# Kernel tuning notes

Measured on AMD Instinct MI355X. Metric: run time of the kernel, lower is better.

Reference implementation:

```python
import jax, jax.numpy as jnp
import numpy as np

B, L, C, H = 1, 2048, 2048, 16
D = C // H
EPS = 1e-6
W0 = 30.0  # SIREN frequency

def rmsnorm(x, w, eps=EPS):
    return x * jax.lax.rsqrt(jnp.mean(x * x, axis=-1, keepdims=True) + eps) * w

def depth_rope(x, depth, base=10000.0):
    # same rotation for all positions, angle set by scalar layer depth
    d = x.shape[-1]
    half = d // 2
    freqs = 1.0 / base ** (jnp.arange(half, dtype=x.dtype) / half)
    ang = depth * freqs
    cos, sin = jnp.cos(ang), jnp.sin(ang)
    x1, x2 = x[..., :half], x[..., half:2 * half]
    return jnp.concatenate([x1 * cos - x2 * sin, x1 * sin + x2 * cos], axis=-1)

def setup_inputs() -> dict:
    key = jax.random.key(0)
    ks = jax.random.split(key, 13)
    s = 1.0 / np.sqrt(C)
    inp = {
        'x':  jax.random.normal(ks[0], (B, L, C), jnp.float32),
        'h0': jax.random.normal(ks[1], (B, L, C), jnp.float32),
        'h1': jax.random.normal(ks[2], (B, L, C), jnp.float32),
        'h2': jax.random.normal(ks[3], (B, L, C), jnp.float32),
        'Wq': jax.random.normal(ks[4], (C, C), jnp.float32) * s,
        'Wk': jax.random.normal(ks[5], (C, C), jnp.float32) * s,
        'Wv': jax.random.normal(ks[6], (C, C), jnp.float32) * s,
        'Wo': jax.random.normal(ks[7], (C, C), jnp.float32) * s,
        'qn_w': jnp.ones((D,), jnp.float32),
        'kn_w': jnp.ones((D,), jnp.float32),
        'on_w': jnp.ones((C,), jnp.float32),
        'sw1': jax.random.normal(ks[8], (1, C), jnp.float32),
        'sb1': jax.random.normal(ks[9], (C,), jnp.float32) * 0.01,
        'sw2': jax.random.normal(ks[10], (C, C), jnp.float32) * s,
        'sb2': jnp.zeros((C,), jnp.float32),
    }
    return inp

def reference(x, h0, h1, h2, Wq, Wk, Wv, Wo, qn_w, kn_w, on_w, sw1, sb1, sw2, sb2):
    history = [h0, h1, h2]
    q_src = history[-1]                      # [B,L,C]
    q_depth = len(history) - 1
    # Q path: proj -> per-head RMSNorm -> depth RoPE
    q = jnp.einsum('blc,oc->blo', q_src, Wq).reshape(B, L, H, D)
    q = depth_rope(rmsnorm(q, qn_w), q_depth)
    # K/V path over prior history entries (each with its own depth)
    k_parts, v_parts = [], []
    for depth_idx, kv in enumerate(history[:-1]):
        k_i = jnp.einsum('blc,oc->blo', kv, Wk).reshape(B, L, H, D)
        v_i = jnp.einsum('blc,oc->blo', kv, Wv).reshape(B, L, H, D)
        k_parts.append(depth_rope(rmsnorm(k_i, kn_w), depth_idx))
        v_parts.append(v_i)
    k = jnp.concatenate(k_parts, axis=1)     # [B,Lkv,H,D]
    v = jnp.concatenate(v_parts, axis=1)
    # full SDPA, default scale D^-0.5
    scores = jnp.einsum('bqhd,bkhd->bhqk', q, k) * (D ** -0.5)
    attn = jax.nn.softmax(scores, axis=-1)
    out = jnp.einsum('bhqk,bkhd->bqhd', attn, v).reshape(B, L, C)
    out = jnp.einsum('blc,oc->blo', out, Wo)
    # SIREN upsample to (L,): target length == L -> identity interpolation
    # plus sine-activated coordinate MLP (implicit positional field)
    coords = jnp.linspace(-1.0, 1.0, L, dtype=x.dtype)[:, None]   # [L,1]
    pos = jnp.sin(W0 * (coords @ sw1 + sb1)) @ sw2 + sb2           # [L,C]
    out = out + pos[None]
    return x + rmsnorm(out, on_w)
```

## Files before the change

### kernel.cpp

```cpp
#include <hip/hip_runtime.h>
#include <hip/hip_fp16.h>

#define LQ 2048
#define CDIM 2048
#define NHEAD 16
#define HDIM 128
#define LKEY 4096

typedef _Float16 f16x8 __attribute__((ext_vector_type(8)));
typedef _Float16 f16x4 __attribute__((ext_vector_type(4)));
typedef float f32x4 __attribute__((ext_vector_type(4)));

#define GLOAD_LDS16(g, s) __builtin_amdgcn_global_load_lds( \
    (const __attribute__((address_space(1))) void*)(g),     \
    (__attribute__((address_space(3))) void*)(s), 16, 0, 0)

#define MFMA16(a, b, c) __builtin_amdgcn_mfma_f32_16x16x32_f16(a, b, c, 0, 0, 0)

__device__ __forceinline__ void storeC(float* p, float v) { *p = v; }
__device__ __forceinline__ void storeC(__half* p, float v) { *p = __float2half(v); }

template <int MODE, typename OutT>
__device__ __forceinline__ void gemm_body(
    __half* smem,
    const __half* __restrict__ A, const __half* __restrict__ B,
    OutT* __restrict__ C, int lda, int ldb, int ldc, int K,
    int bmA, int bmC, int bn,
    const float* __restrict__ wgt, int kmode, float oscale,
    __half* __restrict__ vTo)
{
    __half* lA = smem;
    __half* lB = smem + 8192;
    const int tid  = threadIdx.x;
    const int lane = tid & 63;
    const int wave = tid >> 6;
    const int r = tid >> 3;
    const int g = tid & 7;
    const __half* gA = A + (long)(bmA * 128 + r) * lda + ((g ^ (r & 7)) << 3);
    const __half* gB = B + (long)(bn * 128 + r) * ldb + ((g ^ (r & 7)) << 3);
    __half* lAp = lA + tid * 8;
    __half* lBp = lB + tid * 8;
    const int wr = (wave & 1) << 6;
    const int wc = (wave >> 1) << 6;
    const int l15 = lane & 15, quad = lane >> 4;

    f32x4 acc[4][4] = {};

    for (int kt = 0; kt < K; kt += 64) {
#pragma unroll
        for (int i = 0; i < 4; ++i) {
            GLOAD_LDS16(gA + (long)i * 32 * lda, lAp + i * 2048);
            GLOAD_LDS16(gB + (long)i * 32 * ldb, lBp + i * 2048);
        }
        gA += 64; gB += 64;
        __syncthreads();
#pragma unroll
        for (int kk = 0; kk < 2; ++kk) {
            f16x8 af[4], bfr[4];
#pragma unroll
            for (int mi = 0; mi < 4; ++mi) {
                const int m = wr + mi * 16 + l15;
                const int kg = kk * 4 + quad;
                af[mi] = *(const f16x8*)&lA[m * 64 + ((kg ^ (m & 7)) << 3)];
            }
#pragma unroll
            for (int ni = 0; ni < 4; ++ni) {
                const int n = wc + ni * 16 + l15;
                const int kg = kk * 4 + quad;
                bfr[ni] = *(const f16x8*)&lB[n * 64 + ((kg ^ (n & 7)) << 3)];
            }
#pragma unroll
            for (int mi = 0; mi < 4; ++mi)
#pragma unroll
                for (int ni = 0; ni < 4; ++ni)
                    acc[mi][ni] = MFMA16(af[mi], bfr[ni], acc[mi][ni]);
        }
        __syncthreads();
    }

    if constexpr (MODE == 0) {
        const int row0 = bmC * 128 + wr + quad * 4;
        const int col0 = bn * 128 + wc + l15;
#pragma unroll
        for (int mi = 0; mi < 4; ++mi)
#pragma unroll
            for (int ni = 0; ni < 4; ++ni)
#pragma unroll
                for (int rx = 0; rx < 4; ++rx)
                    storeC(&C[(long)(row0 + mi * 16 + rx) * ldc + col0 + ni * 16],
                           acc[mi][ni][rx]);
    } else if constexpr (MODE == 2) {
#pragma unroll
        for (int mi = 0; mi < 4; ++mi)
#pragma unroll
            for (int ni = 0; ni < 4; ++ni)
#pragma unroll
                for (int rx = 0; rx < 4; ++rx) {
                    const int  d   = (bn - 16) * 128 + wc + ni * 16 + l15;
                    const long key = (long)bmC * 128 + wr + mi * 16 + quad * 4 + rx;
                    vTo[(long)d * LKEY + key] = __float2half(acc[mi][ni][rx]);
                }
    } else {
        __half* sT = smem;
#pragma unroll
        for (int mi = 0; mi < 4; ++mi)
#pragma unroll
            for (int ni = 0; ni < 4; ++ni)
#pragma unroll
                for (int rx = 0; rx < 4; ++rx)
                    sT[(wr + mi * 16 + quad * 4 + rx) * 136 + wc + ni * 16 + l15] =
                        (_Float16)acc[mi][ni][rx];
        __syncthreads();
        const int row = (wave << 5) + (lane >> 1);
        const int c0  = (lane & 1) << 5;
        const __half* rp = sT + row * 136;
        f16x8 L[4], Hh[4];
#pragma unroll
        for (int j8 = 0; j8 < 4; ++j8) {
            L[j8]  = *(const f16x8*)&rp[c0 + j8 * 8];
            Hh[j8] = *(const f16x8*)&rp[c0 + 64 + j8 * 8];
        }
        float ss = 0.f;
#pragma unroll
        for (int j8 = 0; j8 < 4; ++j8)
#pragma unroll
            for (int e = 0; e < 8; ++e) {
                const float a = (float)L[j8][e], b = (float)Hh[j8][e];
                ss += a * a + b * b;
            }
        ss += __shfl_xor(ss, 1);
        const float rn = rsqrtf(ss * (1.0f / 128.0f) + 1e-6f);
        const long grow = (long)bmC * 128 + row;
        const int depth = kmode ? (grow < 2048 ? 0 : 1) : 2;
        union { f16x8 v; _Float16 e[8]; } o1[4], o2[4];
#pragma unroll
        for (int j8 = 0; j8 < 4; ++j8)
#pragma unroll
            for (int e = 0; e < 8; ++e) {
                const int d = c0 + j8 * 8 + e;
                const float x1 = (float)L[j8][e]  * rn * wgt[d];
                const float x2 = (float)Hh[j8][e] * rn * wgt[d + 64];
                const float ang = (float)depth *
                    exp2f(-(float)d * 0.20762050593045702f);
                float sn, cs;
                __sincosf(ang, &sn, &cs);
                o1[j8].e[e] = (_Float16)((x1 * cs - x2 * sn) * oscale);
                o2[j8].e[e] = (_Float16)((x1 * sn + x2 * cs) * oscale);
            }
        __half* op = (__half*)C + grow * ldc + bn * 128;
#pragma unroll
        for (int j8 = 0; j8 < 4; ++j8) {
            *(f16x8*)&op[c0 + j8 * 8]      = o1[j8].v;
            *(f16x8*)&op[c0 + 64 + j8 * 8] = o2[j8].v;
        }
    }
}

__global__ __launch_bounds__(256, 2) void gemm_qkv(
    const __half* __restrict__ A, const __half* __restrict__ Bq,
    const __half* __restrict__ Bkv, __half* __restrict__ Cq,
    __half* __restrict__ Ckv, __half* __restrict__ vT,
    const float* __restrict__ qn_w, const float* __restrict__ kn_w)
{
    __shared__ __align__(16) __half smem[17408];
    const int lin = blockIdx.x;
    if (lin < 1024) {
        const int bm = lin & 31, bn = lin >> 5;
        if (bn < 16)
            gemm_body<1, __half>(smem, A, Bkv, Ckv, 2048, 2048, 4096, 2048,
                                 bm + 16, bm, bn, kn_w, 1, 1.0f, nullptr);
        else
            gemm_body<2, __half>(smem, A, Bkv, Ckv, 2048, 2048, 4096, 2048,
                                 bm + 16, bm, bn, nullptr, 0, 1.0f, vT);
    } else {
        const int l2 = lin - 1024;
        const int bm = l2 & 15, bn = l2 >> 4;
        gemm_body<1, __half>(smem, A, Bq, Cq, 2048, 2048, 2048, 2048,
                             bm, bm, bn, qn_w, 0, 0.12751743f, nullptr);
    }
}

__global__ __launch_bounds__(256, 2) void gemm_sk(
    const __half* __restrict__ A, const __half* __restrict__ B,
    float* __restrict__ C, int lda, int ldb, int ldc, int Khalf)
{
    __shared__ __align__(16) __half smem[16384];
    const int z = blockIdx.z;
    gemm_body<0, float>(smem, A + z * Khalf, B + z * Khalf,
                        C + (long)z * LQ * CDIM,
                        lda, ldb, ldc, Khalf, blockIdx.x, blockIdx.x, blockIdx.y,
                        nullptr, 0, 1.0f, nullptr);
}

__global__ __launch_bounds__(256, 2) void attn_tile(
    const __half* __restrict__ Qf,
    const __half* __restrict__ Kf,
    const __half* __restrict__ Vt,
    float* __restrict__ Opart,
    float* __restrict__ lsum)
{
    __shared__ __align__(16) __half lK[64 * 128];
    __shared__ __align__(16) __half lV[128 * 64];
    __shared__ __align__(16) __half pL[4 * 2 * 16 * 76];

    const int tid  = threadIdx.x;
    const int lane = tid & 63;
    const int wave = tid >> 6;
    const int l15  = lane & 15;
    const int quad = lane >> 4;
    const int lin = blockIdx.y * 16 + blockIdx.x;
    const int hkc = (lin & 7) * 4 + ((lin >> 3) & 3);
    const int qt  = lin >> 5;
    const int h   = hkc >> 1;
    const int kc  = hkc & 1;
    const int q0  = qt * 128 + wave * 32;

    f16x8 aq[2][4];
#pragma unroll
    for (int mt = 0; mt < 2; ++mt)
#pragma unroll
        for (int ks = 0; ks < 4; ++ks)
            aq[mt][ks] = *(const f16x8*)&Qf[(long)(q0 + mt * 16 + l15) * CDIM +
                                            h * HDIM + ks * 32 + quad * 8];

    const int rK = tid >> 4;
    const int gK = tid & 15;
    const __half* srcK = Kf + (long)(kc * 2048 + rK) * 4096 + h * HDIM +
                         ((gK ^ (rK & 15)) << 3);
    const int rV = tid >> 3;
    const int gV = tid & 7;
    const __half* srcV = Vt + (long)(h * HDIM + rV) * (long)LKEY + kc * 2048 +
                         ((gV ^ (rV & 7)) << 3);
    __half* dstK = lK + tid * 8;
    __half* dstV = lV + tid * 8;

    f32x4 accO[2][8] = {};
    f32x4 l_acc[2] = {};

    for (int st = 0; st < 32; ++st) {
#pragma unroll
        for (int i = 0; i < 4; ++i) {
            GLOAD_LDS16(srcK + (long)(st * 64 + i * 16) * 4096, dstK + i * 2048);
            GLOAD_LDS16(srcV + (long)i * 32 * LKEY + st * 64, dstV + i * 2048);
        }
        __syncthreads();
        f32x4 s[2][4];
#pragma unroll
        for (int mt = 0; mt < 2; ++mt)
#pragma unroll
            for (int nt = 0; nt < 4; ++nt)
                s[mt][nt] = (f32x4){-10.f, -10.f, -10.f, -10.f};
#pragma unroll
        for (int nt = 0; nt < 4; ++nt) {
            const int n = nt * 16 + l15;
#pragma unroll
            for (int ks = 0; ks < 4; ++ks) {
                const f16x8 kf = *(const f16x8*)
                    &lK[n * 128 + (((ks * 4 + quad) ^ (n & 15)) << 3)];
                s[0][nt] = MFMA16(aq[0][ks], kf, s[0][nt]);
                s[1][nt] = MFMA16(aq[1][ks], kf, s[1][nt]);
            }
        }
#pragma unroll
        for (int mt = 0; mt < 2; ++mt)
#pragma unroll
            for (int nt = 0; nt < 4; ++nt)
#pragma unroll
                for (int r2 = 0; r2 < 4; ++r2) {
                    const float p = __builtin_amdgcn_exp2f(s[mt][nt][r2]);
                    l_acc[mt][r2] += p;
                    pL[((wave * 2 + mt) * 16 + quad * 4 + r2) * 76 +
                       nt * 16 + l15] = __float2half(p);
                }
        f16x8 ap[2][2];
#pragma unroll
        for (int mt = 0; mt < 2; ++mt) {
            ap[mt][0] = *(const f16x8*)&pL[((wave * 2 + mt) * 16 + l15) * 76 + quad * 8];
            ap[mt][1] = *(const f16x8*)&pL[((wave * 2 + mt) * 16 + l15) * 76 + 32 + quad * 8];
        }
#pragma unroll
        for (int nt2 = 0; nt2 < 8; ++nt2) {
            const int n2 = nt2 * 16 + l15;
            const f16x8 v0 = *(const f16x8*)&lV[n2 * 64 + ((quad ^ (n2 & 7)) << 3)];
            const f16x8 v1 = *(const f16x8*)&lV[n2 * 64 + (((4 + quad) ^ (n2 & 7)) << 3)];
            accO[0][nt2] = MFMA16(ap[0][0], v0, accO[0][nt2]);
            accO[0][nt2] = MFMA16(ap[0][1], v1, accO[0][nt2]);
            accO[1][nt2] = MFMA16(ap[1][0], v0, accO[1][nt2]);
            accO[1][nt2] = MFMA16(ap[1][1], v1, accO[1][nt2]);
        }
        __syncthreads();
    }

#pragma unroll
    for (int mt = 0; mt < 2; ++mt)
#pragma unroll
        for (int r2 = 0; r2 < 4; ++r2) {
            float v = l_acc[mt][r2];
            v += __shfl_xor(v, 1);
            v += __shfl_xor(v, 2);
            v += __shfl_xor(v, 4);
            v += __shfl_xor(v, 8);
            if (l15 == 0)
                atomicAdd(&lsum[h * LQ + q0 + mt * 16 + quad * 4 + r2], v);
        }
    float* Cp = Opart + (long)kc * LQ * CDIM + h * HDIM;
#pragma unroll
    for (int mt = 0; mt < 2; ++mt)
#pragma unroll
        for (int nt2 = 0; nt2 < 8; ++nt2)
#pragma unroll
            for (int rx = 0; rx < 4; ++rx)
                Cp[(long)(q0 + mt * 16 + quad * 4 + rx) * CDIM + nt2 * 16 + l15] =
                    accO[mt][nt2][rx];
}

__global__ __launch_bounds__(256) void merge_o(
    const float* __restrict__ Op, const float* __restrict__ lsum,
    __half* __restrict__ a2)
{
    const int row = blockIdx.x;
    const int c0  = threadIdx.x * 8;
    const float inv = 1.0f / lsum[(c0 >> 7) * LQ + row];
    const float* p0 = Op + (long)row * CDIM + c0;
    const float* p1 = p0 + (long)LQ * CDIM;
    union { f16x8 v; _Float16 e[8]; } o;
#pragma unroll
    for (int j = 0; j < 8; ++j)
        o.e[j] = (_Float16)((p0[j] + p1[j]) * inv);
    *(f16x8*)&a2[(long)row * 4096 + c0] = o.v;
}

__global__ __launch_bounds__(256) void prep_all(
    const float* __restrict__ h2, const float* __restrict__ h0,
    const float* __restrict__ h1, const float* __restrict__ Wq,
    const float* __restrict__ Wk, const float* __restrict__ Wv,
    const float* __restrict__ Wo, const float* __restrict__ sw1,
    const float* __restrict__ sb1, const float* __restrict__ sw2,
    __half* __restrict__ xq, __half* __restrict__ xkv,
    __half* __restrict__ wqh, __half* __restrict__ wkv,
    __half* __restrict__ a2, __half* __restrict__ b2,
    float* __restrict__ lsum)
{
    __shared__ float t[64][65];
    const int blk = blockIdx.x;
    const int tid = threadIdx.x;
    if (blk < 24576) {
        const long i = ((long)blk * 256 + tid) << 2;
        const int chunk = (int)(i >> 22);
        const long off = i & 4194303;
        const float* s; __half* d;
        switch (chunk) {
            case 0:  s = h2; d = xq;            break;
            case 1:  s = h0; d = xkv;           break;
            case 2:  s = h1; d = xkv + 4194304; break;
            case 3:  s = Wq; d = wqh;           break;
            case 4:  s = Wk; d = wkv;           break;
            default: s = Wv; d = wkv + 4194304; break;
        }
        const float4 v = *(const float4*)&s[off];
        f16x4 o;
        o[0] = (_Float16)v.x; o[1] = (_Float16)v.y;
        o[2] = (_Float16)v.z; o[3] = (_Float16)v.w;
        *(f16x4*)&d[off] = o;
    } else if (blk < 28672) {
        const int i = ((blk - 24576) * 256 + tid) << 2;
        const int o = i >> 11, c = i & 2047;
        const float4 v = *(const float4*)&Wo[i];
        f16x4 w4;
        w4[0] = (_Float16)v.x; w4[1] = (_Float16)v.y;
        w4[2] = (_Float16)v.z; w4[3] = (_Float16)v.w;
        *(f16x4*)&b2[((long)o << 12) + c] = w4;
    } else if (blk < 29696) {
        const int lb = blk - 28672;
        const long r0 = (long)(lb & 31) * 64;
        const long c0 = (long)(lb >> 5) * 64;
        const int tj = tid & 63;
        const int ti = tid >> 6;
#pragma unroll
        for (int it = 0; it < 16; ++it) {
            const int i = it * 4 + ti;
            t[i][tj] = sw2[(r0 + i) * 2048 + c0 + tj];
        }
        __syncthreads();
#pragma unroll
        for (int it = 0; it < 16; ++it) {
            const int i = it * 4 + ti;
            b2[(c0 + i) * 4096 + 2048 + r0 + tj] = __float2half(t[tj][i]);
        }
    } else if (blk < 33792) {
        const int i = ((blk - 29696) * 256 + tid) << 2;
        const int l = i >> 11, c = i & 2047;
        const float coord = -1.0f + (2.0f / 2047.0f) * (float)l;
        const float4 w = *(const float4*)&sw1[c];
        const float4 b = *(const float4*)&sb1[c];
        f16x4 o;
        o[0] = (_Float16)__sinf(30.0f * (coord * w.x + b.x));
        o[1] = (_Float16)__sinf(30.0f * (coord * w.y + b.y));
        o[2] = (_Float16)__sinf(30.0f * (coord * w.z + b.z));
        o[3] = (_Float16)__sinf(30.0f * (coord * w.w + b.w));
        *(f16x4*)&a2[((long)l << 12) + 2048 + c] = o;
    } else {
        const int i = ((blk - 33792) * 256 + tid) << 2;
        *(float4*)&lsum[i] = (float4){0.f, 0.f, 0.f, 0.f};
    }
}

__global__ __launch_bounds__(256) void final_norm(
    const float* __restrict__ out2, const float* __restrict__ x,
    const float* __restrict__ sb2, const float* __restrict__ on_w,
    float* __restrict__ y)
{
    const int row = blockIdx.x;
    const float* o0 = out2 + (long)row * CDIM;
    const float* o1 = o0 + (long)LQ * CDIM;
    float4 v[2];
    float ss = 0.f;
#pragma unroll
    for (int i = 0; i < 2; ++i) {
        const int c = threadIdx.x * 4 + i * 1024;
        const float4 a = *(const float4*)&o0[c];
        const float4 b = *(const float4*)&o1[c];
        const float4 s = *(const float4*)&sb2[c];
        float4 tv;
        tv.x = a.x + b.x + s.x; tv.y = a.y + b.y + s.y;
        tv.z = a.z + b.z + s.z; tv.w = a.w + b.w + s.w;
        v[i] = tv;
        ss += tv.x * tv.x + tv.y * tv.y + tv.z * tv.z + tv.w * tv.w;
    }
#pragma unroll
    for (int off = 1; off < 64; off <<= 1) ss += __shfl_xor(ss, off);
    __shared__ float red[4];
    const int lane = threadIdx.x & 63, wv = threadIdx.x >> 6;
    if (lane == 0) red[wv] = ss;
    __syncthreads();
    const float tot = red[0] + red[1] + red[2] + red[3];
    const float rn = rsqrtf(tot * (1.0f / 2048.0f) + 1e-6f);
#pragma unroll
    for (int i = 0; i < 2; ++i) {
        const int c = threadIdx.x * 4 + i * 1024;
        const float4 xr = *(const float4*)&x[(long)row * CDIM + c];
        const float4 wv4 = *(const float4*)&on_w[c];
        float4 o;
        o.x = xr.x + v[i].x * rn * wv4.x;
        o.y = xr.y + v[i].y * rn * wv4.y;
        o.z = xr.z + v[i].z * rn * wv4.z;
        o.w = xr.w + v[i].w * rn * wv4.w;
        *(float4*)&y[(long)row * CDIM + c] = o;
    }
}

extern "C" void kernel_launch(void* const* d_in, const int* in_sizes, int n_in,
                              void* d_out, int out_size, void* d_ws, size_t ws_size,
                              hipStream_t stream) {
    const float* x    = (const float*)d_in[0];
    const float* h0   = (const float*)d_in[1];
    const float* h1   = (const float*)d_in[2];
    const float* h2   = (const float*)d_in[3];
    const float* Wq   = (const float*)d_in[4];
    const float* Wk   = (const float*)d_in[5];
    const float* Wv   = (const float*)d_in[6];
    const float* Wo   = (const float*)d_in[7];
    const float* qn_w = (const float*)d_in[8];
    const float* kn_w = (const float*)d_in[9];
    const float* on_w = (const float*)d_in[10];
    const float* sw1  = (const float*)d_in[11];
    const float* sb1  = (const float*)d_in[12];
    const float* sw2  = (const float*)d_in[13];
    const float* sb2  = (const float*)d_in[14];
    float* y = (float*)d_out;

    const size_t MB = 1ull << 20;
    char* w = (char*)d_ws;
    __half* xq  = (__half*)(w);
    __half* xkv = (__half*)(w + 8 * MB);
    __half* wqh = (__half*)(w + 24 * MB);
    __half* wkv = (__half*)(w + 32 * MB);
    __half* qf  = (__half*)(w + 48 * MB);
    __half* kvf = (__half*)(w + 56 * MB);
    __half* vT  = (__half*)(w + 88 * MB);
    __half* a2  = (__half*)(w + 104 * MB);
    __half* b2  = (__half*)(w + 120 * MB);
    float* lsum  = (float*)(w + 136 * MB);
    float* Opart = (float*)(w);
    float* out2  = (float*)(w);
    (void)in_sizes; (void)n_in; (void)out_size; (void)ws_size;

    prep_all<<<33824, 256, 0, stream>>>(h2, h0, h1, Wq, Wk, Wv, Wo, sw1, sb1,
                                        sw2, xq, xkv, wqh, wkv, a2, b2, lsum);

    gemm_qkv<<<1280, 256, 0, stream>>>(xq, wqh, wkv, qf, kvf, vT, qn_w, kn_w);

    attn_tile<<<dim3(16, 32), 256, 0, stream>>>(qf, kvf, vT, Opart, lsum);
    merge_o<<<2048, 256, 0, stream>>>(Opart, lsum, a2);

    gemm_sk<<<dim3(16, 16, 2), 256, 0, stream>>>(a2, b2, out2, 4096, 4096, 2048, 2048);
    final_norm<<<2048, 256, 0, stream>>>(out2, x, sb2, on_w, y);
}
```

Before: 445.9 us.

## Split QKV GEMM into 256x256-tile KV kernel and separate Q kernel

Replaces the combined 128x128-tile QKV GEMM with a dedicated KV projection kernel. It uses 512 threads, 256x256 output tiles and a 128KB double-buffered LDS pipeline, with per-quarter prefetch, explicit barriers and MFMA priority raising. The intent is more operand reuse per LDS load and better overlap of global-to-LDS loads with MFMA work, one block per CU. The Q projection becomes its own launch, which adds a kernel boundary and gives up the concurrency the merged launch had.

```diff
diff --git a/kernel.cpp b/kernel.cpp
--- a/kernel.cpp
+++ b/kernel.cpp
@@ -26,8 +26,7 @@
     const __half* __restrict__ A, const __half* __restrict__ B,
     OutT* __restrict__ C, int lda, int ldb, int ldc, int K,
     int bmA, int bmC, int bn,
-    const float* __restrict__ wgt, int kmode, float oscale,
-    __half* __restrict__ vTo)
+    const float* __restrict__ wgt, int kmode, float oscale)
 {
     __half* lA = smem;
     __half* lB = smem + 8192;
@@ -89,17 +88,6 @@
                 for (int rx = 0; rx < 4; ++rx)
                     storeC(&C[(long)(row0 + mi * 16 + rx) * ldc + col0 + ni * 16],
                            acc[mi][ni][rx]);
-    } else if constexpr (MODE == 2) {
-#pragma unroll
-        for (int mi = 0; mi < 4; ++mi)
-#pragma unroll
-            for (int ni = 0; ni < 4; ++ni)
-#pragma unroll
-                for (int rx = 0; rx < 4; ++rx) {
-                    const int  d   = (bn - 16) * 128 + wc + ni * 16 + l15;
-                    const long key = (long)bmC * 128 + wr + mi * 16 + quad * 4 + rx;
-                    vTo[(long)d * LKEY + key] = __float2half(acc[mi][ni][rx]);
-                }
     } else {
         __half* sT = smem;
 #pragma unroll
@@ -156,28 +144,162 @@
     }
 }
 
-__global__ __launch_bounds__(256, 2) void gemm_qkv(
+__device__ __forceinline__ void stage_half(
+    const __half* __restrict__ M, long row0, int T, char* lds, int slot, int tid)
+{
+    char* dst = lds + slot * 16384 + tid * 16;
+    const int r = tid >> 3;
+    const int g = tid & 7;
+    const int co = T * 64 + ((g ^ (r & 7)) << 3);
+    GLOAD_LDS16(M + (row0 + r) * 2048 + co, dst);
+    GLOAD_LDS16(M + (row0 + r + 64) * 2048 + co, dst + 8192);
+}
+
+__global__ __launch_bounds__(512, 1) void gemm_kv8(
+    const __half* __restrict__ A,
+    const __half* __restrict__ B,
+    __half* __restrict__ Ckv,
+    __half* __restrict__ vT,
+    const float* __restrict__ kn_w)
+{
+    __shared__ __align__(16) char LDS[131072];
+    const int tid  = threadIdx.x;
+    const int lane = tid & 63;
+    const int wave = tid >> 6;
+    const int wm = wave >> 2;
+    const int wn = wave & 3;
+    const int l15 = lane & 15, quad = lane >> 4;
+    const int bm = blockIdx.x & 15;
+    const int bn = blockIdx.x >> 4;
+    const long arow = (long)bm * 256;
+    const long brow = (long)bn * 256;
+
+    f32x4 acc[8][4] = {};
+
+    stage_half(A, arow,       0, LDS, 0, tid);
+    stage_half(A, arow + 128, 0, LDS, 1, tid);
+    stage_half(B, brow,       0, LDS, 4, tid);
+    stage_half(B, brow + 128, 0, LDS, 5, tid);
+
+    for (int tt = 0; tt < 32; ++tt) {
+        const int buf = tt & 1, sbuf = buf ^ 1;
+        const int Tn = (tt < 31) ? tt + 1 : 31;
+        const __half* As = (const __half*)(LDS + (buf * 2 + wm) * 16384);
+        const __half* Bs = (const __half*)(LDS + (4 + buf * 2 + (wn >> 1)) * 16384);
+        f16x8 bq[4][2];
+#pragma unroll
+        for (int q = 0; q < 4; ++q) {
+            if (q == 0)      stage_half(A, arow,       Tn, LDS, 0 + sbuf * 2, tid);
+            else if (q == 1) stage_half(A, arow + 128, Tn, LDS, 1 + sbuf * 2, tid);
+            else if (q == 2) stage_half(B, brow,       Tn, LDS, 4 + sbuf * 2, tid);
+            else             stage_half(B, brow + 128, Tn, LDS, 5 + sbuf * 2, tid);
+            if (q == 0)
+                asm volatile("s_waitcnt vmcnt(2)" ::: "memory");
+            __builtin_amdgcn_s_barrier();
+            __builtin_amdgcn_sched_barrier(0);
+            if (q == 0) {
+#pragma unroll
+                for (int ni = 0; ni < 4; ++ni) {
+                    const int rb = ((wn & 1) << 6) + ni * 16 + l15;
+#pragma unroll
+                    for (int ks = 0; ks < 2; ++ks)
+                        bq[ni][ks] = *(const f16x8*)
+                            &Bs[rb * 64 + (((ks * 4 + quad) ^ (rb & 7)) << 3)];
+                }
+            }
+            f16x8 av[2][2];
+#pragma unroll
+            for (int m2 = 0; m2 < 2; ++m2) {
+                const int ra = (q * 2 + m2) * 16 + l15;
+#pragma unroll
+                for (int ks = 0; ks < 2; ++ks)
+                    av[m2][ks] = *(const f16x8*)
+                        &As[ra * 64 + (((ks * 4 + quad) ^ (ra & 7)) << 3)];
+            }
+            __builtin_amdgcn_s_setprio(1);
+#pragma unroll
+            for (int m2 = 0; m2 < 2; ++m2)
+#pragma unroll
+                for (int ni = 0; ni < 4; ++ni) {
+                    acc[q * 2 + m2][ni] = MFMA16(av[m2][0], bq[ni][0], acc[q * 2 + m2][ni]);
+                    acc[q * 2 + m2][ni] = MFMA16(av[m2][1], bq[ni][1], acc[q * 2 + m2][ni]);
+                }
+            __builtin_amdgcn_s_setprio(0);
+            __builtin_amdgcn_s_barrier();
+            __builtin_amdgcn_sched_barrier(0);
+        }
+    }
+
+    __syncthreads();
+
+    if (bn < 8) {
+        __half* sT = (__half*)LDS;
+#pragma unroll
+        for (int mi = 0; mi < 8; ++mi)
+#pragma unroll
+            for (int ni = 0; ni < 4; ++ni)
+#pragma unroll
+                for (int rx = 0; rx < 4; ++rx)
+                    sT[(wm * 128 + mi * 16 + quad * 4 + rx) * 256 +
+                       wn * 64 + ni * 16 + l15] = (_Float16)acc[mi][ni][rx];
+        __syncthreads();
+        const int row = tid >> 1;
+        const int hs  = tid & 1;
+        const __half* rp = sT + row * 256 + hs * 128;
+        f16x8 xv[16];
+#pragma unroll
+        for (int j = 0; j < 16; ++j) xv[j] = *(const f16x8*)&rp[j * 8];
+        float ss = 0.f;
+#pragma unroll
+        for (int j = 0; j < 16; ++j)
+#pragma unroll
+            for (int e = 0; e < 8; ++e) {
+                const float v = (float)xv[j][e];
+                ss += v * v;
+            }
+        const float rn = rsqrtf(ss * (1.0f / 128.0f) + 1e-6f);
+        const long R = arow + row;
+        const float depth = (R < 2048) ? 0.f : 1.f;
+        __half* op = Ckv + R * 4096 + bn * 256 + hs * 128;
+#pragma unroll
+        for (int j = 0; j < 8; ++j) {
+            union { f16x8 v; _Float16 e[8]; } o1, o2;
+#pragma unroll
+            for (int e = 0; e < 8; ++e) {
+                const int d = j * 8 + e;
+                const float x1 = (float)xv[j][e]     * rn * kn_w[d];
+                const float x2 = (float)xv[j + 8][e] * rn * kn_w[d + 64];
+                const float ang = depth * exp2f(-(float)d * 0.20762050593045702f);
+                float sn, cs;
+                __sincosf(ang, &sn, &cs);
+                o1.e[e] = (_Float16)(x1 * cs - x2 * sn);
+                o2.e[e] = (_Float16)(x1 * sn + x2 * cs);
+            }
+            *(f16x8*)&op[j * 8]      = o1.v;
+            *(f16x8*)&op[64 + j * 8] = o2.v;
+        }
+    } else {
+#pragma unroll
+        for (int mi = 0; mi < 8; ++mi)
+#pragma unroll
+            for (int ni = 0; ni < 4; ++ni)
+#pragma unroll
+                for (int rx = 0; rx < 4; ++rx) {
+                    const int d = (bn - 8) * 256 + wn * 64 + ni * 16 + l15;
+                    const long key = arow + wm * 128 + mi * 16 + quad * 4 + rx;
+                    vT[(long)d * LKEY + key] = __float2half(acc[mi][ni][rx]);
+                }
+    }
+}
+
+__global__ __launch_bounds__(256, 2) void gemm_q(
     const __half* __restrict__ A, const __half* __restrict__ Bq,
-    const __half* __restrict__ Bkv, __half* __restrict__ Cq,
-    __half* __restrict__ Ckv, __half* __restrict__ vT,
-    const float* __restrict__ qn_w, const float* __restrict__ kn_w)
+    __half* __restrict__ Cq, const float* __restrict__ qn_w)
 {
     __shared__ __align__(16) __half smem[17408];
-    const int lin = blockIdx.x;
-    if (lin < 1024) {
-        const int bm = lin & 31, bn = lin >> 5;
-        if (bn < 16)
-            gemm_body<1, __half>(smem, A, Bkv, Ckv, 2048, 2048, 4096, 2048,
-                                 bm + 16, bm, bn, kn_w, 1, 1.0f, nullptr);
-        else
-            gemm_body<2, __half>(smem, A, Bkv, Ckv, 2048, 2048, 4096, 2048,
-                                 bm + 16, bm, bn, nullptr, 0, 1.0f, vT);
-    } else {
-        const int l2 = lin - 1024;
-        const int bm = l2 & 15, bn = l2 >> 4;
-        gemm_body<1, __half>(smem, A, Bq, Cq, 2048, 2048, 2048, 2048,
-                             bm, bm, bn, qn_w, 0, 0.12751743f, nullptr);
-    }
+    const int bm = blockIdx.x & 15, bn = blockIdx.x >> 4;
+    gemm_body<1, __half>(smem, A, Bq, Cq, 2048, 2048, 2048, 2048,
+                         bm, bm, bn, qn_w, 0, 0.12751743f);
 }
 
 __global__ __launch_bounds__(256, 2) void gemm_sk(
@@ -189,7 +311,7 @@
     gemm_body<0, float>(smem, A + z * Khalf, B + z * Khalf,
                         C + (long)z * LQ * CDIM,
                         lda, ldb, ldc, Khalf, blockIdx.x, blockIdx.x, blockIdx.y,
-                        nullptr, 0, 1.0f, nullptr);
+                        nullptr, 0, 1.0f);
 }
 
 __global__ __launch_bounds__(256, 2) void attn_tile(
@@ -488,7 +610,8 @@
     prep_all<<<33824, 256, 0, stream>>>(h2, h0, h1, Wq, Wk, Wv, Wo, sw1, sb1,
                                         sw2, xq, xkv, wqh, wkv, a2, b2, lsum);
 
-    gemm_qkv<<<1280, 256, 0, stream>>>(xq, wqh, wkv, qf, kvf, vT, qn_w, kn_w);
+    gemm_kv8<<<256, 512, 0, stream>>>(xkv, wkv, kvf, vT, kn_w);
+    gemm_q<<<256, 256, 0, stream>>>(xq, wqh, qf, qn_w);
 
     attn_tile<<<dim3(16, 32), 256, 0, stream>>>(qf, kvf, vT, Opart, lsum);
     merge_o<<<2048, 256, 0, stream>>>(Opart, lsum, a2);
```

Result: faster. 435.6 us (-2.3%).
